# Optimization experiments

Hardware: AMD Instinct MI355X
Metric: run time of the kernel (lower is better)

Reference implementation:

```python
import jax, jax.numpy as jnp
import numpy as np

D_MODEL = 1024
N_HEADS = 16
HEAD_DIM = D_MODEL // N_HEADS
D_FF = 4096
EPS = 1e-5


def _layer_norm(x, gamma, beta):
    mu = jnp.mean(x, axis=-1, keepdims=True)
    var = jnp.var(x, axis=-1, keepdims=True)
    return (x - mu) * jax.lax.rsqrt(var + EPS) * gamma + beta


def setup_inputs() -> dict:
    key = jax.random.key(0)
    ks = jax.random.split(key, 16)
    B, T, S = 2, 2048, 2048
    s = 1.0 / np.sqrt(D_MODEL)
    inp = {
        "tgt": jax.random.normal(ks[0], (B, T, D_MODEL), jnp.float32),
        "memory": jax.random.normal(ks[1], (B, S, D_MODEL), jnp.float32),
        "wq": jax.random.normal(ks[2], (D_MODEL, D_MODEL), jnp.float32) * s,
        "bq": jnp.zeros((D_MODEL,), jnp.float32),
        "wk": jax.random.normal(ks[3], (D_MODEL, D_MODEL), jnp.float32) * s,
        "bk": jnp.zeros((D_MODEL,), jnp.float32),
        "wv": jax.random.normal(ks[4], (D_MODEL, D_MODEL), jnp.float32) * s,
        "bv": jnp.zeros((D_MODEL,), jnp.float32),
        "wo": jax.random.normal(ks[5], (D_MODEL, D_MODEL), jnp.float32) * s,
        "bo": jnp.zeros((D_MODEL,), jnp.float32),
        "w1": jax.random.normal(ks[6], (D_MODEL, D_FF), jnp.float32) * s,
        "b1": jnp.zeros((D_FF,), jnp.float32),
        "w2": jax.random.normal(ks[7], (D_FF, D_MODEL), jnp.float32) * (1.0 / np.sqrt(D_FF)),
        "b2": jnp.zeros((D_MODEL,), jnp.float32),
        "g1": jnp.ones((D_MODEL,), jnp.float32),
        "be1": jnp.zeros((D_MODEL,), jnp.float32),
        "g2": jnp.ones((D_MODEL,), jnp.float32),
        "be2": jnp.zeros((D_MODEL,), jnp.float32),
    }
    return inp


def reference(tgt, memory, wq, bq, wk, bk, wv, bv, wo, bo, w1, b1, w2, b2, g1, be1, g2, be2):
    B, T, _ = tgt.shape
    S = memory.shape[1]
    scale = HEAD_DIM ** -0.5
    # projections -> [B, H, L, Dh]
    Q = (tgt @ wq + bq).reshape(B, T, N_HEADS, HEAD_DIM).transpose(0, 2, 1, 3)
    K = (memory @ wk + bk).reshape(B, S, N_HEADS, HEAD_DIM).transpose(0, 2, 1, 3)
    V = (memory @ wv + bv).reshape(B, S, N_HEADS, HEAD_DIM).transpose(0, 2, 1, 3)
    scores = jnp.einsum("bhtd,bhsd->bhts", Q, K) * scale
    attn = jax.nn.softmax(scores, axis=-1)  # dropout=0 (eval)
    ctx = jnp.einsum("bhts,bhsd->bhtd", attn, V)
    ctx = ctx.transpose(0, 2, 1, 3).reshape(B, T, D_MODEL)
    attn_out = ctx @ wo + bo
    # post-norm residual blocks
    x = _layer_norm(tgt + attn_out, g1, be1)
    ff = jax.nn.relu(x @ w1 + b1) @ w2 + b2
    out = _layer_norm(x + ff, g2, be2)
    return out
```

## Files before the change

### kernel.cpp

```cpp
#include <hip/hip_runtime.h>


typedef unsigned short u16;
typedef __attribute__((ext_vector_type(8))) short bvec8;
typedef __attribute__((ext_vector_type(4))) float fvec4;

#define MFMA16(a, b, c) __builtin_amdgcn_mfma_f32_16x16x32_bf16((a), (b), (c), 0, 0, 0)

__device__ __forceinline__ u16 f2b(float f) {
  union { float f; unsigned u; } x; x.f = f;
  unsigned u = x.u;
  return (u16)((u + 0x7FFFu + ((u >> 16) & 1u)) >> 16);
}
__device__ __forceinline__ u16 f2b_t(float f) {
  union { float f; unsigned u; } x; x.f = f;
  return (u16)(x.u >> 16);
}
__device__ __forceinline__ void gl_lds16(const u16* g, u16* lds) {
  __builtin_amdgcn_global_load_lds(
      (const __attribute__((address_space(1))) void*)g,
      (__attribute__((address_space(3))) void*)lds, 16, 0, 0);
}

__global__ __launch_bounds__(256) void k_pre(
    const float* __restrict__ tgt, const float* __restrict__ mem,
    const float* __restrict__ wq, const float* __restrict__ wk,
    const float* __restrict__ wv, const float* __restrict__ wo,
    const float* __restrict__ w1, const float* __restrict__ w2,
    u16* __restrict__ tgt_b, u16* __restrict__ mem_b,
    u16* __restrict__ wqT, u16* __restrict__ wkvT, u16* __restrict__ woT,
    u16* __restrict__ w1T, u16* __restrict__ w2T) {
  __shared__ float t[32][33];
  int bb = blockIdx.x;
  if (bb < 8192) {
    const float* in = (bb < 4096) ? tgt : mem;
    u16* outp = (bb < 4096) ? tgt_b : mem_b;
    int i = (bb & 4095) * 256 + threadIdx.x;
    float4 v = ((const float4*)in)[i];
    ushort4 o;
    o.x = f2b(v.x); o.y = f2b(v.y); o.z = f2b(v.z); o.w = f2b(v.w);
    ((ushort4*)outp)[i] = o;
    return;
  }
  int b = bb - 8192;
  const float* W; u16* WT; int K, N, bx, by;
  if (b < 4096) {
    int m = b >> 10, tt = b & 1023;
    bx = tt & 31; by = tt >> 5; K = 1024; N = 1024;
    W = (m == 0) ? wq : (m == 1) ? wk : (m == 2) ? wv : wo;
    WT = (m == 0) ? wqT : (m == 1) ? wkvT : (m == 2) ? wkvT + 1024 * 1024 : woT;
  } else if (b < 8192) {
    int tt = b - 4096; bx = tt & 127; by = tt >> 7; K = 1024; N = 4096;
    W = w1; WT = w1T;
  } else {
    int tt = b - 8192; bx = tt & 31; by = tt >> 5; K = 4096; N = 1024;
    W = w2; WT = w2T;
  }
  int tx = threadIdx.x & 31, ty = threadIdx.x >> 5;
  int n0 = bx * 32, k0 = by * 32;
#pragma unroll
  for (int i = 0; i < 4; i++)
    t[ty + i * 8][tx] = W[(size_t)(k0 + ty + i * 8) * N + n0 + tx];
  __syncthreads();
#pragma unroll
  for (int i = 0; i < 4; i++)
    WT[(size_t)(n0 + ty + i * 8) * K + k0 + tx] = f2b(t[tx][ty + i * 8]);
}

__global__ __launch_bounds__(256, 4) void k_qkv(
    const u16* __restrict__ tgt_b, const u16* __restrict__ mem_b,
    const u16* __restrict__ wqT, const u16* __restrict__ wkvT,
    const float* __restrict__ bq, const float* __restrict__ bk,
    const float* __restrict__ bv,
    u16* __restrict__ Qb, u16* __restrict__ Kb, u16* __restrict__ Vtb) {
  __shared__ u16 S[256 * 64];
  const int tid = threadIdx.x, w = tid >> 6, lane = tid & 63;
  const int q = lane >> 4, l = lane & 15;
  const bool isQ = blockIdx.x < 256;
  const int id = isQ ? blockIdx.x : blockIdx.x - 256;
  const int nx = isQ ? 8 : 16;
  const int m0 = (id / nx) * 128, n0 = (id % nx) * 128;
  const u16* A = isQ ? tgt_b : mem_b;
  const u16* BT = isQ ? wqT : wkvT;
  const int wm = (w >> 1) * 64, wn = (w & 1) * 64;
  const int rowin = lane >> 3, grp = lane & 7;
  const int gcol = ((grp + rowin) & 7) * 8;
  const int kc0 = ((q + 8 - (l & 7)) & 7) * 8;
  const int kc1 = ((q + 12 - (l & 7)) & 7) * 8;
  const u16* gp[8];
  u16* lp[8];
#pragma unroll
  for (int c = 0; c < 8; c++) {
    int r0 = (w * 8 + c) * 8;
    gp[c] = (r0 < 128) ? A + (size_t)(m0 + r0 + rowin) * 1024 + gcol
                       : BT + (size_t)(n0 + r0 - 128 + rowin) * 1024 + gcol;
    lp[c] = &S[r0 * 64];
  }
  fvec4 acc[4][4] = {};
#pragma unroll 1
  for (int k0 = 0; k0 < 1024; k0 += 64) {
#pragma unroll
    for (int c = 0; c < 8; c++) gl_lds16(gp[c] + k0, lp[c]);
    __syncthreads();
#pragma unroll
    for (int kh = 0; kh < 2; kh++) {
      const int kc = kh ? kc1 : kc0;
      bvec8 af[4], bf[4];
#pragma unroll
      for (int i = 0; i < 4; i++) {
        af[i] = *(const bvec8*)&S[(wm + 16 * i + l) * 64 + kc];
        bf[i] = *(const bvec8*)&S[(128 + wn + 16 * i + l) * 64 + kc];
      }
#pragma unroll
      for (int i = 0; i < 4; i++)
#pragma unroll
        for (int j = 0; j < 4; j++)
          acc[i][j] = MFMA16(af[i], bf[j], acc[i][j]);
    }
    __syncthreads();
  }
#pragma unroll
  for (int mi = 0; mi < 4; mi++)
#pragma unroll
    for (int ni = 0; ni < 4; ni++) {
      int row = m0 + wm + mi * 16 + q * 4;
      int col = n0 + wn + ni * 16 + l;
      if (isQ) {
        float bvv = bq[col];
#pragma unroll
        for (int r = 0; r < 4; r++)
          Qb[(size_t)(row + r) * 1024 + col] = f2b((acc[mi][ni][r] + bvv) * 0.125f);
      } else if (col < 1024) {
        float bvv = bk[col];
#pragma unroll
        for (int r = 0; r < 4; r++)
          Kb[(size_t)(row + r) * 1024 + col] = f2b(acc[mi][ni][r] + bvv);
      } else {
        int vcol = col - 1024;
        float bvv = bv[vcol];
        int b = row >> 11, s = row & 2047;
        int h = vcol >> 6, d = vcol & 63;
        ushort4 o;
        o.x = f2b(acc[mi][ni][0] + bvv);
        o.y = f2b(acc[mi][ni][1] + bvv);
        o.z = f2b(acc[mi][ni][2] + bvv);
        o.w = f2b(acc[mi][ni][3] + bvv);
        *(ushort4*)&Vtb[((size_t)(b * 16 + h) * 64 + d) * 2048 + s] = o;
      }
    }
}

template <int TM, int TN>
__global__ __launch_bounds__(256, 4) void k_gemm(
    const u16* __restrict__ A, const u16* __restrict__ BT,
    const float* __restrict__ bias, const float* __restrict__ resid,
    float* __restrict__ outF, u16* __restrict__ outB,
    int M, int N, int Kstride, int Klen, float scale, int flags) {
  constexpr int WM = TM / 2, WN = TN / 2;
  constexpr int MI = WM / 16, NI = WN / 16;
  constexpr int NCALL = (TM + TN) / 32;
  __shared__ u16 S[(TM + TN) * 64];
  const int tid = threadIdx.x, w = tid >> 6, lane = tid & 63;
  const int q = lane >> 4, l = lane & 15;
  const int m0 = blockIdx.y * TM, n0 = blockIdx.x * TN;
  const int kbeg = blockIdx.z * Klen;
  const int wm = (w >> 1) * WM, wn = (w & 1) * WN;
  const int rowin = lane >> 3, grp = lane & 7;
  const int gcol = ((grp + rowin) & 7) * 8;
  const int kc0 = ((q + 8 - (l & 7)) & 7) * 8;
  const int kc1 = ((q + 12 - (l & 7)) & 7) * 8;
  const u16* gp[NCALL];
  u16* lp[NCALL];
#pragma unroll
  for (int c = 0; c < NCALL; c++) {
    int r0 = (w * NCALL + c) * 8;
    gp[c] = (r0 < TM) ? A + (size_t)(m0 + r0 + rowin) * Kstride + kbeg + gcol
                      : BT + (size_t)(n0 + r0 - TM + rowin) * Kstride + kbeg + gcol;
    lp[c] = &S[r0 * 64];
  }
  fvec4 acc[MI][NI] = {};
#pragma unroll 1
  for (int k0 = 0; k0 < Klen; k0 += 64) {
#pragma unroll
    for (int c = 0; c < NCALL; c++) gl_lds16(gp[c] + k0, lp[c]);
    __syncthreads();
#pragma unroll
    for (int kh = 0; kh < 2; kh++) {
      const int kc = kh ? kc1 : kc0;
      bvec8 af[MI], bf[NI];
#pragma unroll
      for (int i = 0; i < MI; i++)
        af[i] = *(const bvec8*)&S[(wm + 16 * i + l) * 64 + kc];
#pragma unroll
      for (int j = 0; j < NI; j++)
        bf[j] = *(const bvec8*)&S[(TM + wn + 16 * j + l) * 64 + kc];
#pragma unroll
      for (int i = 0; i < MI; i++)
#pragma unroll
        for (int j = 0; j < NI; j++)
          acc[i][j] = MFMA16(af[i], bf[j], acc[i][j]);
    }
    __syncthreads();
  }
  if (flags & 16) {
    float* po = outF + (size_t)blockIdx.z * M * N;
#pragma unroll
    for (int mi = 0; mi < MI; mi++)
#pragma unroll
      for (int ni = 0; ni < NI; ni++) {
        int row = m0 + wm + mi * 16 + q * 4;
        int col = n0 + wn + ni * 16 + l;
#pragma unroll
        for (int r = 0; r < 4; r++)
          po[(size_t)(row + r) * N + col] = acc[mi][ni][r];
      }
    return;
  }
#pragma unroll
  for (int mi = 0; mi < MI; mi++)
#pragma unroll
    for (int ni = 0; ni < NI; ni++) {
      int row = m0 + wm + mi * 16 + q * 4;
      int col = n0 + wn + ni * 16 + l;
      float bvv = bias[col];
#pragma unroll
      for (int r = 0; r < 4; r++) {
        float v = (acc[mi][ni][r] + bvv) * scale;
        if (flags & 1) v = fmaxf(v, 0.0f);
        size_t idx = (size_t)(row + r) * N + col;
        if (flags & 8) v += resid[idx];
        if (flags & 2) outB[idx] = f2b(v);
        if (flags & 4) outF[idx] = v;
      }
    }
}

__global__ __launch_bounds__(256, 4) void k_attn(
    const u16* __restrict__ Q, const u16* __restrict__ Kb,
    const u16* __restrict__ Vt, float* __restrict__ opart,
    float* __restrict__ lpart) {
  __shared__ u16 Ks[64 * 64];
  __shared__ u16 Vs[64 * 64];
  __shared__ u16 Ps[4][2][16 * 72];
  const int tid = threadIdx.x, w = tid >> 6, lane = tid & 63;
  const int q = lane >> 4, l = lane & 15;
  const int blk = blockIdx.x;
  const int bh = blk >> 4, tb = blk & 15;
  const int b = bh >> 4, h = bh & 15;
  const int t0 = tb * 128 + w * 32;
  const int sbeg = blockIdx.y * 1024;
  float* op = opart + (size_t)blockIdx.y * 4096 * 1024;
  float* lp = lpart + (size_t)blockIdx.y * 4096 * 16;
  const u16* Qp = Q + (size_t)(b * 2048 + t0) * 1024 + h * 64;
  const u16* Kp = Kb + (size_t)(b * 2048) * 1024 + h * 64;
  const u16* Vp = Vt + (size_t)bh * 64 * 2048;
  const int rowin = lane >> 3, grp = lane & 7;
  const int gcol = ((grp + rowin) & 7) * 8;
  const int kc0 = ((q + 8 - (l & 7)) & 7) * 8;
  const int kc1 = ((q + 12 - (l & 7)) & 7) * 8;
  bvec8 aQ[2][2];
#pragma unroll
  for (int ti = 0; ti < 2; ti++)
#pragma unroll
    for (int kh = 0; kh < 2; kh++)
      aQ[ti][kh] = *(const bvec8*)&Qp[(size_t)(ti * 16 + l) * 1024 + kh * 32 + q * 8];
  fvec4 o[2][4] = {};
  float ls[2][4] = {};
#pragma unroll 1
  for (int s0 = sbeg; s0 < sbeg + 1024; s0 += 64) {
    gl_lds16(Kp + (size_t)(s0 + w * 8 + rowin) * 1024 + gcol, &Ks[(w * 8) * 64]);
    gl_lds16(Kp + (size_t)(s0 + 32 + w * 8 + rowin) * 1024 + gcol, &Ks[(32 + w * 8) * 64]);
    gl_lds16(Vp + (size_t)(w * 8 + rowin) * 2048 + s0 + gcol, &Vs[(w * 8) * 64]);
    gl_lds16(Vp + (size_t)(32 + w * 8 + rowin) * 2048 + s0 + gcol, &Vs[(32 + w * 8) * 64]);
    __syncthreads();
    fvec4 sc[2][4];
#pragma unroll
    for (int ti = 0; ti < 2; ti++)
#pragma unroll
      for (int ss = 0; ss < 4; ss++) sc[ti][ss] = (fvec4){0.f, 0.f, 0.f, 0.f};
#pragma unroll
    for (int ss = 0; ss < 4; ss++) {
      const int ro = (ss * 16 + l) * 64;
      bvec8 kf0 = *(const bvec8*)&Ks[ro + kc0];
      bvec8 kf1 = *(const bvec8*)&Ks[ro + kc1];
#pragma unroll
      for (int ti = 0; ti < 2; ti++) {
        sc[ti][ss] = MFMA16(aQ[ti][0], kf0, sc[ti][ss]);
        sc[ti][ss] = MFMA16(aQ[ti][1], kf1, sc[ti][ss]);
      }
    }
#pragma unroll
    for (int ti = 0; ti < 2; ti++)
#pragma unroll
      for (int ss = 0; ss < 4; ss++)
#pragma unroll
        for (int r = 0; r < 4; r++) {
          float p = __expf(sc[ti][ss][r]);
          ls[ti][r] += p;
          Ps[w][ti][(q * 4 + r) * 72 + ss * 16 + l] = f2b_t(p);
        }
    asm volatile("s_waitcnt lgkmcnt(0)" ::: "memory");
    bvec8 bV[4][2];
#pragma unroll
    for (int dt = 0; dt < 4; dt++) {
      const int ro = (dt * 16 + l) * 64;
      bV[dt][0] = *(const bvec8*)&Vs[ro + kc0];
      bV[dt][1] = *(const bvec8*)&Vs[ro + kc1];
    }
#pragma unroll
    for (int ti = 0; ti < 2; ti++) {
      bvec8 aP0 = *(const bvec8*)&Ps[w][ti][l * 72 + q * 8];
      bvec8 aP1 = *(const bvec8*)&Ps[w][ti][l * 72 + 32 + q * 8];
#pragma unroll
      for (int dt = 0; dt < 4; dt++) {
        o[ti][dt] = MFMA16(aP0, bV[dt][0], o[ti][dt]);
        o[ti][dt] = MFMA16(aP1, bV[dt][1], o[ti][dt]);
      }
    }
    __syncthreads();
  }
#pragma unroll
  for (int ti = 0; ti < 2; ti++)
#pragma unroll
    for (int r = 0; r < 4; r++) {
      float s = ls[ti][r];
      s += __shfl_xor(s, 1, 64);
      s += __shfl_xor(s, 2, 64);
      s += __shfl_xor(s, 4, 64);
      s += __shfl_xor(s, 8, 64);
      int trow = b * 2048 + t0 + ti * 16 + q * 4 + r;
      if (l == 0) lp[trow * 16 + h] = s;
#pragma unroll
      for (int dt = 0; dt < 4; dt++)
        op[(size_t)trow * 1024 + h * 64 + dt * 16 + l] = o[ti][dt][r];
    }
}

__global__ __launch_bounds__(256) void k_actx(const float* __restrict__ opart,
                                              const float* __restrict__ lpart,
                                              u16* __restrict__ ctx) {
  int row = blockIdx.x, c0 = threadIdx.x * 4;
  int h = c0 >> 6;
  float lsum = lpart[row * 16 + h] + lpart[4096 * 16 + row * 16 + h];
  float inv = 1.0f / lsum;
  float4 a = *(const float4*)&opart[(size_t)row * 1024 + c0];
  float4 b = *(const float4*)&opart[(size_t)4096 * 1024 + (size_t)row * 1024 + c0];
  ushort4 o;
  o.x = f2b((a.x + b.x) * inv);
  o.y = f2b((a.y + b.y) * inv);
  o.z = f2b((a.z + b.z) * inv);
  o.w = f2b((a.w + b.w) * inv);
  *(ushort4*)&ctx[(size_t)row * 1024 + c0] = o;
}

__global__ __launch_bounds__(256) void k_lnp(
    const float* __restrict__ parts, int nparts,
    const float* __restrict__ bias, const float* __restrict__ resid,
    const float* __restrict__ g, const float* __restrict__ be,
    float* __restrict__ xf, u16* __restrict__ xb) {
  __shared__ float sm[8];
  int row = blockIdx.x, tid = threadIdx.x;
  size_t base = (size_t)row * 1024;
  const size_t pstride = (size_t)4096 * 1024;
  float v[4], s = 0.f, ss = 0.f;
#pragma unroll
  for (int j = 0; j < 4; j++) {
    int c = tid + j * 256;
    float acc = bias[c] + resid[base + c];
    for (int z = 0; z < nparts; z++) acc += parts[z * pstride + base + c];
    v[j] = acc;
    s += acc; ss += acc * acc;
  }
#pragma unroll
  for (int off = 32; off; off >>= 1) {
    s += __shfl_down(s, off, 64);
    ss += __shfl_down(ss, off, 64);
  }
  int w = tid >> 6;
  if ((tid & 63) == 0) { sm[w] = s; sm[4 + w] = ss; }
  __syncthreads();
  float S = sm[0] + sm[1] + sm[2] + sm[3];
  float SS = sm[4] + sm[5] + sm[6] + sm[7];
  float mean = S * (1.0f / 1024.0f);
  float var = SS * (1.0f / 1024.0f) - mean * mean;
  float rstd = rsqrtf(var + 1e-5f);
#pragma unroll
  for (int j = 0; j < 4; j++) {
    int c = tid + j * 256;
    float o = (v[j] - mean) * rstd * g[c] + be[c];
    xf[base + c] = o;
    if (xb) xb[base + c] = f2b(o);
  }
}

extern "C" void kernel_launch(void* const* d_in, const int* in_sizes, int n_in,
                              void* d_out, int out_size, void* d_ws, size_t ws_size,
                              hipStream_t stream) {
  (void)in_sizes; (void)n_in; (void)out_size; (void)ws_size;
  const float* tgt = (const float*)d_in[0];
  const float* mem = (const float*)d_in[1];
  const float* wq  = (const float*)d_in[2];
  const float* bq  = (const float*)d_in[3];
  const float* wk  = (const float*)d_in[4];
  const float* bk  = (const float*)d_in[5];
  const float* wv  = (const float*)d_in[6];
  const float* bv  = (const float*)d_in[7];
  const float* wo  = (const float*)d_in[8];
  const float* bo  = (const float*)d_in[9];
  const float* w1  = (const float*)d_in[10];
  const float* b1  = (const float*)d_in[11];
  const float* w2  = (const float*)d_in[12];
  const float* b2  = (const float*)d_in[13];
  const float* g1  = (const float*)d_in[14];
  const float* be1 = (const float*)d_in[15];
  const float* g2  = (const float*)d_in[16];
  const float* be2 = (const float*)d_in[17];
  float* out = (float*)d_out;

  char* ws = (char*)d_ws;
  size_t off = 0;
  auto take = [&](size_t bytes) { char* p = ws + off; off += bytes; return p; };
  const size_t MB = 1024 * 1024;
  u16* tgt_b = (u16*)take(8 * MB);
  u16* mem_b = (u16*)take(8 * MB);
  u16* wqT   = (u16*)take(2 * MB);
  u16* wkvT  = (u16*)take(4 * MB);
  u16* woT   = (u16*)take(2 * MB);
  u16* w1T   = (u16*)take(8 * MB);
  u16* w2T   = (u16*)take(8 * MB);
  u16* Qb    = (u16*)take(8 * MB);
  u16* Kb    = (u16*)take(8 * MB);
  u16* Vtb   = (u16*)take(8 * MB);
  u16* ctx   = (u16*)take(8 * MB);
  float* opart = (float*)take(32 * MB);
  float* opj   = (float*)take(32 * MB);
  float* lpart = (float*)take(1 * MB);
  float* xf  = (float*)take(16 * MB);
  u16* xb    = (u16*)take(8 * MB);
  u16* hbuf  = Qb;
  float* fp2 = opart;

  k_pre<<<20480, 256, 0, stream>>>(tgt, mem, wq, wk, wv, wo, w1, w2,
                                   tgt_b, mem_b, wqT, wkvT, woT, w1T, w2T);
  k_qkv<<<768, 256, 0, stream>>>(tgt_b, mem_b, wqT, wkvT, bq, bk, bv,
                                 Qb, Kb, Vtb);
  k_attn<<<dim3(512, 2), 256, 0, stream>>>(Qb, Kb, Vtb, opart, lpart);
  k_actx<<<4096, 256, 0, stream>>>(opart, lpart, ctx);
  k_gemm<64, 128><<<dim3(8, 64, 1), 256, 0, stream>>>(
      ctx, woT, nullptr, nullptr, opj, nullptr,
      4096, 1024, 1024, 1024, 1.0f, 16);
  k_lnp<<<4096, 256, 0, stream>>>(opj, 1, bo, tgt, g1, be1, xf, xb);
  k_gemm<128, 128><<<dim3(32, 32), 256, 0, stream>>>(
      xb, w1T, b1, nullptr, nullptr, hbuf,
      4096, 4096, 1024, 1024, 1.0f, 1 | 2);
  k_gemm<64, 128><<<dim3(8, 64, 2), 256, 0, stream>>>(
      hbuf, w2T, nullptr, nullptr, fp2, nullptr,
      4096, 1024, 4096, 2048, 1.0f, 16);
  k_lnp<<<4096, 256, 0, stream>>>(fp2, 2, b2, xf, g2, be2, out, nullptr);
}
```

Baseline: 383.1 us.

## Double-buffer K/V in attention and keep P in registers via permlane swaps

The attention kernel now double-buffers the K/V LDS tiles, issuing the next tile's async global-to-LDS loads right after the barrier so they overlap compute, and drops one of the two barriers per iteration. It computes S transposed (K as the A operand), so exponentials can be packed to bf16 with v_cvt_pk and rearranged with permlane32/16 swaps straight into PV MFMA operands. This removes the P round-trip through LDS and its wait. Block indices are also remapped to group heads differently, and outputs are written as vec4 stores. In exchange, the K/V LDS footprint doubles and the code relies on gfx950-specific permlane and conversion instructions.

Result: no change. 384.6 us (+0.4%).

```diff
diff --git a/kernel.cpp b/kernel.cpp
--- a/kernel.cpp
+++ b/kernel.cpp
@@ -4,6 +4,7 @@
 typedef unsigned short u16;
 typedef __attribute__((ext_vector_type(8))) short bvec8;
 typedef __attribute__((ext_vector_type(4))) float fvec4;
+typedef __attribute__((ext_vector_type(4))) unsigned uvec4;
 
 #define MFMA16(a, b, c) __builtin_amdgcn_mfma_f32_16x16x32_bf16((a), (b), (c), 0, 0, 0)
 
@@ -12,10 +13,14 @@
   unsigned u = x.u;
   return (u16)((u + 0x7FFFu + ((u >> 16) & 1u)) >> 16);
 }
-__device__ __forceinline__ u16 f2b_t(float f) {
-  union { float f; unsigned u; } x; x.f = f;
-  return (u16)(x.u >> 16);
-}
+__device__ __forceinline__ unsigned cvtpk(float lo, float hi) {
+  unsigned r;
+  asm("v_cvt_pk_bf16_f32 %0, %1, %2" : "=v"(r) : "v"(lo), "v"(hi));
+  return r;
+}
+#define PLSWAP32(a, b) asm("v_permlane32_swap_b32 %0, %1" : "+v"(a), "+v"(b))
+#define PLSWAP16(a, b) asm("v_permlane16_swap_b32 %0, %1" : "+v"(a), "+v"(b))
+
 __device__ __forceinline__ void gl_lds16(const u16* g, u16* lds) {
   __builtin_amdgcn_global_load_lds(
       (const __attribute__((address_space(1))) void*)g,
@@ -239,12 +244,12 @@
     const u16* __restrict__ Q, const u16* __restrict__ Kb,
     const u16* __restrict__ Vt, float* __restrict__ opart,
     float* __restrict__ lpart) {
-  __shared__ u16 Ks[64 * 64];
-  __shared__ u16 Vs[64 * 64];
-  __shared__ u16 Ps[4][2][16 * 72];
+  __shared__ u16 Ks[2][64 * 64];
+  __shared__ u16 Vs[2][64 * 64];
   const int tid = threadIdx.x, w = tid >> 6, lane = tid & 63;
   const int q = lane >> 4, l = lane & 15;
-  const int blk = blockIdx.x;
+  const int bx = blockIdx.x;
+  const int blk = (bx & 7) * 64 + (bx >> 3);
   const int bh = blk >> 4, tb = blk & 15;
   const int b = bh >> 4, h = bh & 15;
   const int t0 = tb * 128 + w * 32;
@@ -265,75 +270,81 @@
     for (int kh = 0; kh < 2; kh++)
       aQ[ti][kh] = *(const bvec8*)&Qp[(size_t)(ti * 16 + l) * 1024 + kh * 32 + q * 8];
   fvec4 o[2][4] = {};
-  float ls[2][4] = {};
+  float ls[2] = {0.f, 0.f};
+  auto stage = [&](int bb, int sv) {
+    gl_lds16(Kp + (size_t)(sv + w * 8 + rowin) * 1024 + gcol, &Ks[bb][(w * 8) * 64]);
+    gl_lds16(Kp + (size_t)(sv + 32 + w * 8 + rowin) * 1024 + gcol, &Ks[bb][(32 + w * 8) * 64]);
+    gl_lds16(Vp + (size_t)(w * 8 + rowin) * 2048 + sv + gcol, &Vs[bb][(w * 8) * 64]);
+    gl_lds16(Vp + (size_t)(32 + w * 8 + rowin) * 2048 + sv + gcol, &Vs[bb][(32 + w * 8) * 64]);
+  };
+  stage(0, sbeg);
+  int cur = 0;
 #pragma unroll 1
   for (int s0 = sbeg; s0 < sbeg + 1024; s0 += 64) {
-    gl_lds16(Kp + (size_t)(s0 + w * 8 + rowin) * 1024 + gcol, &Ks[(w * 8) * 64]);
-    gl_lds16(Kp + (size_t)(s0 + 32 + w * 8 + rowin) * 1024 + gcol, &Ks[(32 + w * 8) * 64]);
-    gl_lds16(Vp + (size_t)(w * 8 + rowin) * 2048 + s0 + gcol, &Vs[(w * 8) * 64]);
-    gl_lds16(Vp + (size_t)(32 + w * 8 + rowin) * 2048 + s0 + gcol, &Vs[(32 + w * 8) * 64]);
     __syncthreads();
-    fvec4 sc[2][4];
-#pragma unroll
-    for (int ti = 0; ti < 2; ti++)
-#pragma unroll
-      for (int ss = 0; ss < 4; ss++) sc[ti][ss] = (fvec4){0.f, 0.f, 0.f, 0.f};
+    if (s0 + 64 < sbeg + 1024) stage(cur ^ 1, s0 + 64);
+    const u16* KsC = Ks[cur];
+    const u16* VsC = Vs[cur];
+    unsigned pw[2][4][2];
 #pragma unroll
     for (int ss = 0; ss < 4; ss++) {
       const int ro = (ss * 16 + l) * 64;
-      bvec8 kf0 = *(const bvec8*)&Ks[ro + kc0];
-      bvec8 kf1 = *(const bvec8*)&Ks[ro + kc1];
+      bvec8 kf0 = *(const bvec8*)&KsC[ro + kc0];
+      bvec8 kf1 = *(const bvec8*)&KsC[ro + kc1];
 #pragma unroll
       for (int ti = 0; ti < 2; ti++) {
-        sc[ti][ss] = MFMA16(aQ[ti][0], kf0, sc[ti][ss]);
-        sc[ti][ss] = MFMA16(aQ[ti][1], kf1, sc[ti][ss]);
+        fvec4 sc = {0.f, 0.f, 0.f, 0.f};
+        sc = MFMA16(kf0, aQ[ti][0], sc);
+        sc = MFMA16(kf1, aQ[ti][1], sc);
+        float p0 = __expf(sc[0]), p1 = __expf(sc[1]);
+        float p2 = __expf(sc[2]), p3 = __expf(sc[3]);
+        ls[ti] += (p0 + p1) + (p2 + p3);
+        pw[ti][ss][0] = cvtpk(p0, p1);
+        pw[ti][ss][1] = cvtpk(p2, p3);
       }
     }
 #pragma unroll
     for (int ti = 0; ti < 2; ti++)
 #pragma unroll
-      for (int ss = 0; ss < 4; ss++)
-#pragma unroll
-        for (int r = 0; r < 4; r++) {
-          float p = __expf(sc[ti][ss][r]);
-          ls[ti][r] += p;
-          Ps[w][ti][(q * 4 + r) * 72 + ss * 16 + l] = f2b_t(p);
+      for (int b4 = 0; b4 < 2; b4++)
+#pragma unroll
+        for (int r2 = 0; r2 < 2; r2++) {
+          PLSWAP32(pw[ti][2 * b4][r2], pw[ti][2 * b4 + 1][r2]);
+          PLSWAP16(pw[ti][2 * b4][r2], pw[ti][2 * b4 + 1][r2]);
         }
-    asm volatile("s_waitcnt lgkmcnt(0)" ::: "memory");
-    bvec8 bV[4][2];
+    bvec8 bP[2][2];
+#pragma unroll
+    for (int ti = 0; ti < 2; ti++)
+#pragma unroll
+      for (int kh = 0; kh < 2; kh++) {
+        uvec4 t = {pw[ti][2 * kh][0], pw[ti][2 * kh][1],
+                   pw[ti][2 * kh + 1][0], pw[ti][2 * kh + 1][1]};
+        bP[ti][kh] = __builtin_bit_cast(bvec8, t);
+      }
 #pragma unroll
     for (int dt = 0; dt < 4; dt++) {
       const int ro = (dt * 16 + l) * 64;
-      bV[dt][0] = *(const bvec8*)&Vs[ro + kc0];
-      bV[dt][1] = *(const bvec8*)&Vs[ro + kc1];
-    }
-#pragma unroll
-    for (int ti = 0; ti < 2; ti++) {
-      bvec8 aP0 = *(const bvec8*)&Ps[w][ti][l * 72 + q * 8];
-      bvec8 aP1 = *(const bvec8*)&Ps[w][ti][l * 72 + 32 + q * 8];
-#pragma unroll
-      for (int dt = 0; dt < 4; dt++) {
-        o[ti][dt] = MFMA16(aP0, bV[dt][0], o[ti][dt]);
-        o[ti][dt] = MFMA16(aP1, bV[dt][1], o[ti][dt]);
-      }
-    }
-    __syncthreads();
-  }
-#pragma unroll
-  for (int ti = 0; ti < 2; ti++)
-#pragma unroll
-    for (int r = 0; r < 4; r++) {
-      float s = ls[ti][r];
-      s += __shfl_xor(s, 1, 64);
-      s += __shfl_xor(s, 2, 64);
-      s += __shfl_xor(s, 4, 64);
-      s += __shfl_xor(s, 8, 64);
-      int trow = b * 2048 + t0 + ti * 16 + q * 4 + r;
-      if (l == 0) lp[trow * 16 + h] = s;
-#pragma unroll
-      for (int dt = 0; dt < 4; dt++)
-        op[(size_t)trow * 1024 + h * 64 + dt * 16 + l] = o[ti][dt][r];
-    }
+      bvec8 v0 = *(const bvec8*)&VsC[ro + kc0];
+      bvec8 v1 = *(const bvec8*)&VsC[ro + kc1];
+#pragma unroll
+      for (int ti = 0; ti < 2; ti++) {
+        o[ti][dt] = MFMA16(v0, bP[ti][0], o[ti][dt]);
+        o[ti][dt] = MFMA16(v1, bP[ti][1], o[ti][dt]);
+      }
+    }
+    cur ^= 1;
+  }
+#pragma unroll
+  for (int ti = 0; ti < 2; ti++) {
+    float s = ls[ti];
+    s += __shfl_xor(s, 16, 64);
+    s += __shfl_xor(s, 32, 64);
+    int trow = b * 2048 + t0 + ti * 16 + l;
+    if (q == 0) lp[trow * 16 + h] = s;
+#pragma unroll
+    for (int dt = 0; dt < 4; dt++)
+      *(fvec4*)&op[(size_t)trow * 1024 + h * 64 + dt * 16 + q * 4] = o[ti][dt];
+  }
 }
 
 __global__ __launch_bounds__(256) void k_actx(const float* __restrict__ opart,
```
